# Performance work log

Measured on AMD Instinct MI355X. Metric: run time of the kernel, lower is better.

Reference implementation:

```python
import jax, jax.numpy as jnp
import numpy as np

N, E, G = 100000, 1600000, 64
IN_DIM, EMB, HID, HEADS, OUT = 128, 128, 32, 4, 64
CAT = HID * HEADS  # 128
EPS = 1e-5
SLOPE = 0.2


def gat_conv(x, src, dst, W, a_src, a_dst, bias):
    # x: [N, F_in]; W: [HEADS*HID, F_in]; a_*: [1, HEADS, HID]; bias: [HEADS*HID]
    h = (x @ W.T).reshape(N, HEADS, HID)
    s_src = (h * a_src).sum(-1)  # [N, HEADS]
    s_dst = (h * a_dst).sum(-1)
    e = jax.nn.leaky_relu(s_src[src] + s_dst[dst], SLOPE)  # [Etot, HEADS]
    m = jax.ops.segment_max(e, dst, num_segments=N)
    p = jnp.exp(e - m[dst])
    denom = jax.ops.segment_sum(p, dst, num_segments=N)
    alpha = p / denom[dst]  # softmax over incoming edges per dst node
    out = jax.ops.segment_sum(h[src] * alpha[:, :, None], dst, num_segments=N)
    return out.reshape(N, CAT) + bias


def graph_norm(x, batch, w, b, mean_scale):
    cnt = jax.ops.segment_sum(jnp.ones((N,), x.dtype), batch, num_segments=G)[:, None]
    mean = jax.ops.segment_sum(x, batch, num_segments=G) / cnt  # [G, C]
    sub = x - mean_scale * mean[batch]
    var = jax.ops.segment_sum(sub * sub, batch, num_segments=G) / cnt
    inv = 1.0 / jnp.sqrt(var + EPS)
    return w * sub * inv[batch] + b


def setup_inputs() -> dict:
    key = jax.random.key(0)
    ks = jax.random.split(key, 20)
    g = lambda k, shape, s: jax.random.normal(k, shape, dtype=jnp.float32) * s
    inp = {
        'x': g(ks[0], (N, IN_DIM), 1.0),
        'edge_index': jax.random.randint(ks[1], (2, E), 0, N, dtype=jnp.int64 if jax.config.read('jax_enable_x64') else jnp.int32),
        'batch': jnp.sort(jax.random.randint(ks[2], (N,), 0, G)),
        'enc_w': g(ks[3], (EMB, IN_DIM), 0.08),
        'enc_b': jnp.zeros((EMB,), jnp.float32),
        'w1': g(ks[4], (HEADS * HID, EMB), 0.08),
        'att_src1': g(ks[5], (1, HEADS, HID), 0.15),
        'att_dst1': g(ks[6], (1, HEADS, HID), 0.15),
        'b1': jnp.zeros((CAT,), jnp.float32),
        'n1_w': jnp.ones((CAT,), jnp.float32),
        'n1_b': jnp.zeros((CAT,), jnp.float32),
        'n1_ms': jnp.ones((CAT,), jnp.float32),
        'w2': g(ks[7], (HEADS * HID, CAT), 0.08),
        'att_src2': g(ks[8], (1, HEADS, HID), 0.15),
        'att_dst2': g(ks[9], (1, HEADS, HID), 0.15),
        'b2': jnp.zeros((CAT,), jnp.float32),
        'n2_w': jnp.ones((CAT,), jnp.float32),
        'n2_b': jnp.zeros((CAT,), jnp.float32),
        'n2_ms': jnp.ones((CAT,), jnp.float32),
        'fc_w': g(ks[10], (OUT, CAT), 0.08),
        'fc_b': jnp.zeros((OUT,), jnp.float32),
    }
    return inp


def reference(x, edge_index, batch, enc_w, enc_b, w1, att_src1, att_dst1, b1,
              n1_w, n1_b, n1_ms, w2, att_src2, att_dst2, b2, n2_w, n2_b, n2_ms,
              fc_w, fc_b):
    # PyG GATConv adds self-loops by default
    loops = jnp.arange(N, dtype=edge_index.dtype)
    src = jnp.concatenate([edge_index[0], loops])
    dst = jnp.concatenate([edge_index[1], loops])

    h = x @ enc_w.T + enc_b
    h = jax.nn.elu(gat_conv(h, src, dst, w1, att_src1, att_dst1, b1))
    h = graph_norm(h, batch, n1_w, n1_b, n1_ms)  # dropout = identity (eval)
    h = jax.nn.elu(gat_conv(h, src, dst, w2, att_src2, att_dst2, b2))
    h = graph_norm(h, batch, n2_w, n2_b, n2_ms)
    pooled = jax.ops.segment_max(h, batch, num_segments=G)  # global_max_pool
    return pooled @ fc_w.T + fc_b  # out_dim != 1 -> no sigmoid
```

## Files before the change

kernel.cpp:

```cpp
#include <hip/hip_runtime.h>
#include <hip/hip_bf16.h>

#define SLOPE 0.2f
#define EPS_GN 1e-5f
#define APITCH 136
#define NBUCK 391

typedef __attribute__((ext_vector_type(8))) short bfrag;
typedef __attribute__((ext_vector_type(4))) float ffrag;

__device__ __forceinline__ float lrelu(float v) { return v > 0.f ? v : SLOPE * v; }
__device__ __forceinline__ unsigned int flipf(float x) {
    unsigned int u = __float_as_uint(x);
    return (u & 0x80000000u) ? ~u : (u | 0x80000000u);
}
__device__ __forceinline__ float unflipf(unsigned int u) {
    return __uint_as_float((u & 0x80000000u) ? (u & 0x7fffffffu) : ~u);
}
__device__ __forceinline__ short f2bs(float v) {
    __hip_bfloat16 h = __float2bfloat16(v);
    return *reinterpret_cast<short*>(&h);
}
__device__ __forceinline__ float bs2f(short s) {
    __hip_bfloat16 h = *reinterpret_cast<__hip_bfloat16*>(&s);
    return __bfloat162float(h);
}
__device__ __forceinline__ float blo(unsigned int u) { return __uint_as_float(u << 16); }
__device__ __forceinline__ float bhi(unsigned int u) { return __uint_as_float(u & 0xffff0000u); }

__global__ void zero_kernel(float* __restrict__ p, int n) {
    int i = blockIdx.x * 256 + threadIdx.x;
    if (i < n) p[i] = 0.f;
}

__global__ void prep_weights(const float* __restrict__ enc_w,
                             const float* __restrict__ enc_b,
                             const float* __restrict__ w1,
                             const float* __restrict__ w2,
                             unsigned short* __restrict__ WT1b,
                             unsigned short* __restrict__ WT2b,
                             float* __restrict__ bc1, float* __restrict__ bc2) {
    int c = blockIdx.x;
    int k = threadIdx.x;
    __shared__ float w1row[128];
    w1row[k] = w1[c * 128 + k];
    __syncthreads();
    float acc = 0.f;
    for (int j = 0; j < 128; ++j)
        acc = fmaf(w1row[j], enc_w[j * 128 + k], acc);
    WT1b[c * 128 + k] = (unsigned short)f2bs(acc);
    WT2b[c * 128 + k] = (unsigned short)f2bs(w2[c * 128 + k]);
    if (k == 0) {
        float b = 0.f;
        for (int j = 0; j < 128; ++j) b += w1row[j] * enc_b[j];
        bc1[c] = b;
        bc2[c] = 0.f;
    }
}


__global__ void __launch_bounds__(256) bucket_hist(const int* __restrict__ ei,
                                                   int* __restrict__ bhist, int E, int N) {
    __shared__ int h[NBUCK];
    for (int i = threadIdx.x; i < NBUCK; i += 256) h[i] = 0;
    __syncthreads();
    int base = blockIdx.x * 4096;
#pragma unroll
    for (int s = 0; s < 16; ++s) {
        int e = base + s * 256 + threadIdx.x;
        if (e < E + N) {
            int dst = (e < E) ? ei[E + e] : (e - E);
            atomicAdd(&h[dst >> 8], 1);
        }
    }
    __syncthreads();
    for (int i = threadIdx.x; i < NBUCK; i += 256)
        if (h[i]) atomicAdd(&bhist[i], h[i]);
}

__global__ void bucket_scan(const int* __restrict__ bhist,
                            int* __restrict__ bbase, int* __restrict__ bcur) {
    __shared__ int sh[512];
    int t = threadIdx.x;
    int v = (t < NBUCK) ? bhist[t] : 0;
    sh[t] = v;
    __syncthreads();
    for (int off = 1; off < 512; off <<= 1) {
        int add = (t >= off) ? sh[t - off] : 0;
        __syncthreads();
        sh[t] += add;
        __syncthreads();
    }
    if (t < NBUCK) {
        bbase[t] = sh[t] - v;
        bcur[t] = sh[t] - v;
    }
}

__global__ void __launch_bounds__(256) bucket_scatter(const int* __restrict__ ei,
                                                      int* __restrict__ bcur,
                                                      unsigned int* __restrict__ staging,
                                                      int E, int N) {
    __shared__ int h[NBUCK];
    __shared__ int lb[NBUCK];
    for (int i = threadIdx.x; i < NBUCK; i += 256) h[i] = 0;
    __syncthreads();
    int base = blockIdx.x * 4096;
    int srcv[16], dstv[16];
#pragma unroll
    for (int s = 0; s < 16; ++s) {
        int e = base + s * 256 + threadIdx.x;
        srcv[s] = -1;
        if (e < E + N) {
            srcv[s] = (e < E) ? ei[e] : (e - E);
            dstv[s] = (e < E) ? ei[E + e] : (e - E);
            atomicAdd(&h[dstv[s] >> 8], 1);
        }
    }
    __syncthreads();
    for (int i = threadIdx.x; i < NBUCK; i += 256) {
        int c = h[i];
        lb[i] = c ? atomicAdd(&bcur[i], c) : 0;
        h[i] = 0;
    }
    __syncthreads();
#pragma unroll
    for (int s = 0; s < 16; ++s) {
        if (srcv[s] >= 0) {
            int b = dstv[s] >> 8;
            int slot = atomicAdd(&h[b], 1);
            staging[lb[b] + slot] = ((unsigned int)srcv[s] << 8) | (unsigned int)(dstv[s] & 255);
        }
    }
}

__global__ void __launch_bounds__(256) bucket_deg(const unsigned int* __restrict__ staging,
                                                  const int* __restrict__ bbase,
                                                  const int* __restrict__ bcur,
                                                  int* __restrict__ deg, int N) {
    int b = blockIdx.x;
    __shared__ int h[256];
    h[threadIdx.x] = 0;
    __syncthreads();
    int s0 = bbase[b], s1 = bcur[b];
    for (int j = s0 + threadIdx.x; j < s1; j += 256)
        atomicAdd(&h[staging[j] & 255], 1);
    __syncthreads();
    int node = b * 256 + threadIdx.x;
    if (node < N) deg[node] = h[threadIdx.x];
}

__global__ void scan_block_sums(const int* __restrict__ deg, int* __restrict__ part, int N) {
    __shared__ int sh[256];
    int t = threadIdx.x;
    int i = blockIdx.x * 256 + t;
    sh[t] = (i < N) ? deg[i] : 0;
    __syncthreads();
    for (int off = 128; off; off >>= 1) {
        if (t < off) sh[t] += sh[t + off];
        __syncthreads();
    }
    if (t == 0) part[blockIdx.x] = sh[0];
}

__global__ void scan_partials(int* __restrict__ part, int nb) {
    __shared__ int sh[1024];
    int t = threadIdx.x;
    int v = (t < nb) ? part[t] : 0;
    sh[t] = v;
    __syncthreads();
    for (int off = 1; off < 1024; off <<= 1) {
        int add = (t >= off) ? sh[t - off] : 0;
        __syncthreads();
        sh[t] += add;
        __syncthreads();
    }
    if (t < nb) part[t] = sh[t] - v;
}

__global__ void scan_write(const int* __restrict__ deg, const int* __restrict__ part,
                           int* __restrict__ row, int N, int Etot) {
    __shared__ int sh[256];
    int t = threadIdx.x;
    int i = blockIdx.x * 256 + t;
    int v = (i < N) ? deg[i] : 0;
    sh[t] = v;
    __syncthreads();
    for (int off = 1; off < 256; off <<= 1) {
        int add = (t >= off) ? sh[t - off] : 0;
        __syncthreads();
        sh[t] += add;
        __syncthreads();
    }
    int excl = sh[t] - v + part[blockIdx.x];
    if (i < N) row[i] = excl;
    if (i == 0 && blockIdx.x == 0) row[N] = Etot;
}

__global__ void __launch_bounds__(256) bucket_csr(const unsigned int* __restrict__ staging,
                                                  const int* __restrict__ bbase,
                                                  const int* __restrict__ bcur,
                                                  const int* __restrict__ rowp,
                                                  int* __restrict__ esrc, int N) {
    int b = blockIdx.x;
    __shared__ int cur[256];
    int node = b * 256 + threadIdx.x;
    cur[threadIdx.x] = (node < N) ? rowp[node] : 0;
    __syncthreads();
    int s0 = bbase[b], s1 = bcur[b];
    for (int j = s0 + threadIdx.x; j < s1; j += 256) {
        unsigned int p = staging[j];
        int pos = atomicAdd(&cur[p & 255], 1);
        esrc[pos] = (int)(p >> 8);
    }
}

__global__ void __launch_bounds__(256) gemm_mfma(
    const void* __restrict__ Ain, const unsigned short* __restrict__ WTb,
    const float* __restrict__ bias, const float* __restrict__ att_src,
    const float* __restrict__ att_dst, const int* __restrict__ batch,
    const float* __restrict__ Ac, const float* __restrict__ Bc,
    unsigned int* __restrict__ H, float* __restrict__ ssrc, float* __restrict__ sdst, int N) {
    __shared__ short Bsh[128 * APITCH];
    __shared__ short Ash[64 * APITCH];
    __shared__ float asrc_s[128], adst_s[128], bias_s[128];
    int tid = threadIdx.x;
    int base = blockIdx.x * 64;

    for (int idx = tid; idx < 2048; idx += 256) {
        int c = idx >> 4, k8 = (idx & 15) * 8;
        uint4 wv = ((const uint4*)WTb)[idx];
        *(uint4*)&Bsh[c * APITCH + k8] = wv;
    }
    if (Ac == nullptr) {
        const float* A = (const float*)Ain;
        for (int idx = tid; idx < 2048; idx += 256) {
            int nl = idx >> 5, k4 = (idx & 31) * 4;
            int node = base + nl;
            float4 v = make_float4(0.f, 0.f, 0.f, 0.f);
            if (node < N) v = ((const float4*)A)[node * 32 + (idx & 31)];
            *(short4*)&Ash[nl * APITCH + k4] =
                make_short4(f2bs(v.x), f2bs(v.y), f2bs(v.z), f2bs(v.w));
        }
    } else {
        const uint4* A4 = (const uint4*)Ain;
        for (int idx = tid; idx < 1024; idx += 256) {
            int nl = idx >> 4, u4 = idx & 15, k8 = u4 * 8;
            int node = base + nl;
            short o[8] = {0, 0, 0, 0, 0, 0, 0, 0};
            if (node < N) {
                uint4 hb = A4[node * 16 + u4];
                int g = batch[node];
                float4 a0 = *(const float4*)&Ac[g * 128 + k8];
                float4 a1 = *(const float4*)&Ac[g * 128 + k8 + 4];
                float4 b0 = *(const float4*)&Bc[g * 128 + k8];
                float4 b1 = *(const float4*)&Bc[g * 128 + k8 + 4];
                o[0] = f2bs(fmaf(blo(hb.x), a0.x, b0.x));
                o[1] = f2bs(fmaf(bhi(hb.x), a0.y, b0.y));
                o[2] = f2bs(fmaf(blo(hb.y), a0.z, b0.z));
                o[3] = f2bs(fmaf(bhi(hb.y), a0.w, b0.w));
                o[4] = f2bs(fmaf(blo(hb.z), a1.x, b1.x));
                o[5] = f2bs(fmaf(bhi(hb.z), a1.y, b1.y));
                o[6] = f2bs(fmaf(blo(hb.w), a1.z, b1.z));
                o[7] = f2bs(fmaf(bhi(hb.w), a1.w, b1.w));
            }
            *(bfrag*)&Ash[nl * APITCH + k8] = *(bfrag*)o;
        }
    }
    if (tid < 128) {
        asrc_s[tid] = att_src[tid];
        adst_s[tid] = att_dst[tid];
        bias_s[tid] = bias[tid];
    }
    __syncthreads();

    int w = tid >> 6, lane = tid & 63, col = lane & 15, quad = lane >> 4;
    int rowBase = w * 16;

    bfrag afr[4];
#pragma unroll
    for (int s = 0; s < 4; ++s)
        afr[s] = *(const bfrag*)&Ash[(rowBase + col) * APITCH + s * 32 + quad * 8];

    ffrag acc[8];
#pragma unroll
    for (int t = 0; t < 8; ++t) acc[t] = (ffrag){0.f, 0.f, 0.f, 0.f};

#pragma unroll
    for (int t = 0; t < 8; ++t) {
#pragma unroll
        for (int s = 0; s < 4; ++s) {
            bfrag bfr = *(const bfrag*)&Bsh[(t * 16 + col) * APITCH + s * 32 + quad * 8];
            acc[t] = __builtin_amdgcn_mfma_f32_16x16x32_bf16(afr[s], bfr, acc[t], 0, 0, 0);
        }
    }

#pragma unroll
    for (int t = 0; t < 8; ++t) {
        int ch = t * 16 + col;
        float bv = bias_s[ch];
#pragma unroll
        for (int r = 0; r < 4; ++r)
            Ash[(rowBase + quad * 4 + r) * APITCH + ch] = f2bs(acc[t][r] + bv);
    }
    __syncthreads();

    float2 av = make_float2(asrc_s[lane * 2], asrc_s[lane * 2 + 1]);
    float2 dv = make_float2(adst_s[lane * 2], adst_s[lane * 2 + 1]);
    for (int r = 0; r < 16; ++r) {
        int node = base + rowBase + r;
        unsigned int hb = *(const unsigned int*)&Ash[(rowBase + r) * APITCH + lane * 2];
        float hx = blo(hb);
        float hy = bhi(hb);
        float vs = hx * av.x + hy * av.y;
        float vd = hx * dv.x + hy * dv.y;
#pragma unroll
        for (int off = 8; off; off >>= 1) {
            vs += __shfl_xor(vs, off, 16);
            vd += __shfl_xor(vd, off, 16);
        }
        if (node < N) {
            H[node * 64 + lane] = hb;
            if ((lane & 15) == 0) {
                int h = lane >> 4;
                ssrc[node * 4 + h] = vs;
                sdst[node * 4 + h] = vd;
            }
        }
    }
}

__global__ void __launch_bounds__(256) agg_kernel(
    const int* __restrict__ row, const int* __restrict__ esrc,
    const float* __restrict__ ssrc, const float* __restrict__ sdst,
    const uint4* __restrict__ H4, const float* __restrict__ bias,
    uint4* __restrict__ out, int N) {
    int n = (blockIdx.x * 256 + threadIdx.x) >> 6;
    int lane = threadIdx.x & 63;
    if (n >= N) return;
    int slot = lane >> 4, li = lane & 15, head = li >> 2;
    int beg = row[n], end = row[n + 1];
    float sdh = sdst[n * 4 + head];

    float num[8] = {0.f, 0.f, 0.f, 0.f, 0.f, 0.f, 0.f, 0.f};
    float den = 0.f;
    for (int e = beg + slot; e < end; e += 4) {
        int s = esrc[e];
        float al = __expf(lrelu(ssrc[s * 4 + head] + sdh));
        uint4 hb = H4[s * 16 + li];
        den += al;
        num[0] = fmaf(al, blo(hb.x), num[0]);
        num[1] = fmaf(al, bhi(hb.x), num[1]);
        num[2] = fmaf(al, blo(hb.y), num[2]);
        num[3] = fmaf(al, bhi(hb.y), num[3]);
        num[4] = fmaf(al, blo(hb.z), num[4]);
        num[5] = fmaf(al, bhi(hb.z), num[5]);
        num[6] = fmaf(al, blo(hb.w), num[6]);
        num[7] = fmaf(al, bhi(hb.w), num[7]);
    }
    den += __shfl_xor(den, 16);
    den += __shfl_xor(den, 32);
#pragma unroll
    for (int j = 0; j < 8; ++j) {
        num[j] += __shfl_xor(num[j], 16);
        num[j] += __shfl_xor(num[j], 32);
    }
    if (slot == 0) {
        float rh = 1.f / den;
        int c0 = li * 8;
        unsigned int o[4];
#pragma unroll
        for (int p = 0; p < 4; ++p) {
            float v0 = fmaf(num[2 * p], rh, bias[c0 + 2 * p]);
            float v1 = fmaf(num[2 * p + 1], rh, bias[c0 + 2 * p + 1]);
            v0 = v0 > 0.f ? v0 : __expf(v0) - 1.f;
            v1 = v1 > 0.f ? v1 : __expf(v1) - 1.f;
            o[p] = ((unsigned int)(unsigned short)f2bs(v0)) |
                   (((unsigned int)(unsigned short)f2bs(v1)) << 16);
        }
        out[n * 16 + li] = make_uint4(o[0], o[1], o[2], o[3]);
    }
}

__global__ void norm_stats(const short* __restrict__ X, const int* __restrict__ batch,
                           float* __restrict__ gsum, float* __restrict__ gsq,
                           int* __restrict__ gcnt, int N, int countFlag) {
    int c = threadIdx.x;
    int base = blockIdx.x * 64;
    if (base >= N) return;
    int end = min(base + 64, N);
    int cur = batch[base];
    float s = 0.f, q = 0.f;
    int cnt = 0;
    for (int n = base; n < end; ++n) {
        int g = batch[n];
        if (g != cur) {
            atomicAdd(&gsum[cur * 128 + c], s);
            atomicAdd(&gsq[cur * 128 + c], q);
            if (c == 0 && countFlag) atomicAdd(&gcnt[cur], cnt);
            s = 0.f; q = 0.f; cnt = 0; cur = g;
        }
        float v = bs2f(X[n * 128 + c]);
        s += v;
        q += v * v;
        ++cnt;
    }
    atomicAdd(&gsum[cur * 128 + c], s);
    atomicAdd(&gsq[cur * 128 + c], q);
    if (c == 0 && countFlag) atomicAdd(&gcnt[cur], cnt);
}

__global__ void norm_coef(const float* __restrict__ gsum, const float* __restrict__ gsq,
                          const int* __restrict__ gcnt,
                          const float* __restrict__ w, const float* __restrict__ b,
                          const float* __restrict__ ms,
                          float* __restrict__ Ac, float* __restrict__ Bc) {
    int g = blockIdx.x, c = threadIdx.x;
    int i = g * 128 + c;
    float cntv = (float)gcnt[g];
    if (cntv < 0.5f) { Ac[i] = 0.f; Bc[i] = 0.f; return; }
    float mean = gsum[i] / cntv;
    float msv = ms[c];
    float var = gsq[i] / cntv - msv * (2.f - msv) * mean * mean;
    var = fmaxf(var, 0.f);
    float inv = rsqrtf(var + EPS_GN);
    float wv = w[c];
    Ac[i] = wv * inv;
    Bc[i] = b[c] - msv * mean * wv * inv;
}

__global__ void norm_pool(const short* __restrict__ X, const int* __restrict__ batch,
                          const float* __restrict__ Ac, const float* __restrict__ Bc,
                          unsigned int* __restrict__ pool, int N) {
    int c = threadIdx.x;
    int base = blockIdx.x * 64;
    if (base >= N) return;
    int end = min(base + 64, N);
    int cur = batch[base];
    float mx = -3e38f;
    for (int n = base; n < end; ++n) {
        int g = batch[n];
        if (g != cur) {
            atomicMax(&pool[cur * 128 + c], flipf(mx));
            mx = -3e38f;
            cur = g;
        }
        float v = fmaf(bs2f(X[n * 128 + c]), Ac[g * 128 + c], Bc[g * 128 + c]);
        mx = fmaxf(mx, v);
    }
    atomicMax(&pool[cur * 128 + c], flipf(mx));
}

__global__ void fc_kernel(const unsigned int* __restrict__ pool,
                          const float* __restrict__ fcw,
                          const float* __restrict__ fcb,
                          float* __restrict__ out) {
    int g = blockIdx.x, o = threadIdx.x;
    __shared__ float p[128];
    p[o] = unflipf(pool[g * 128 + o]);
    p[o + 64] = unflipf(pool[g * 128 + 64 + o]);
    __syncthreads();
    float acc = fcb[o];
    for (int k = 0; k < 128; ++k)
        acc = fmaf(p[k], fcw[o * 128 + k], acc);
    out[g * 64 + o] = acc;
}

extern "C" void kernel_launch(void* const* d_in, const int* in_sizes, int n_in,
                              void* d_out, int out_size, void* d_ws, size_t ws_size,
                              hipStream_t stream) {
    const float* x     = (const float*)d_in[0];
    const int* ei      = (const int*)d_in[1];
    const int* batch   = (const int*)d_in[2];
    const float* enc_w = (const float*)d_in[3];
    const float* enc_b = (const float*)d_in[4];
    const float* w1    = (const float*)d_in[5];
    const float* as1   = (const float*)d_in[6];
    const float* ad1   = (const float*)d_in[7];
    const float* b1    = (const float*)d_in[8];
    const float* n1w   = (const float*)d_in[9];
    const float* n1b   = (const float*)d_in[10];
    const float* n1ms  = (const float*)d_in[11];
    const float* w2    = (const float*)d_in[12];
    const float* as2   = (const float*)d_in[13];
    const float* ad2   = (const float*)d_in[14];
    const float* b2    = (const float*)d_in[15];
    const float* n2w   = (const float*)d_in[16];
    const float* n2b   = (const float*)d_in[17];
    const float* n2ms  = (const float*)d_in[18];
    const float* fcw   = (const float*)d_in[19];
    const float* fcb   = (const float*)d_in[20];
    float* out = (float*)d_out;

    int N = in_sizes[2];
    int E = in_sizes[1] / 2;
    int Etot = E + N;

    char* ws = (char*)d_ws;
    size_t off = 0;
    auto take = [&](size_t bytes) {
        char* p = ws + off;
        off = (off + bytes + 255) & ~(size_t)255;
        return p;
    };
    unsigned short* WT1b = (unsigned short*)take(128 * 128 * 2);
    unsigned short* WT2b = (unsigned short*)take(128 * 128 * 2);
    float* bc1 = (float*)take(512);
    float* bc2 = (float*)take(512);
    float* ssrc = (float*)take((size_t)N * 16);
    float* sdst = (float*)take((size_t)N * 16);
    int* rowp   = (int*)take((size_t)(N + 1) * 4);
    int* part   = (int*)take(4096 * 4);
    int* esrc   = (int*)take((size_t)Etot * 4);
    unsigned int* staging = (unsigned int*)take((size_t)Etot * 4);
    int* bbase  = (int*)take(512 * 4);
    int* bcur   = (int*)take(512 * 4);
    int* deg    = (int*)take((size_t)N * 4);
    unsigned int* H = (unsigned int*)take((size_t)N * 256);
    unsigned int* AG = (unsigned int*)take((size_t)N * 256);
    float* Ac   = (float*)take(64 * 128 * 4);
    float* Bc   = (float*)take(64 * 128 * 4);
    size_t zbeg = off;
    int* bhist   = (int*)take(512 * 4);
    float* gsumA = (float*)take(64 * 128 * 4);
    float* gsqA  = (float*)take(64 * 128 * 4);
    float* gsumB = (float*)take(64 * 128 * 4);
    float* gsqB  = (float*)take(64 * 128 * 4);
    int* gcnt    = (int*)take(256);
    unsigned int* pool = (unsigned int*)take(64 * 128 * 4);
    size_t zend = off;
    if (off > ws_size) return;

    int zn = (int)((zend - zbeg) / 4);
    int NB = (N + 255) / 256;
    int EB = (Etot + 4095) / 4096;

    zero_kernel<<<(zn + 255) / 256, 256, 0, stream>>>((float*)(ws + zbeg), zn);
    prep_weights<<<128, 128, 0, stream>>>(enc_w, enc_b, w1, w2, WT1b, WT2b, bc1, bc2);

    bucket_hist<<<EB, 256, 0, stream>>>(ei, bhist, E, N);
    bucket_scan<<<1, 512, 0, stream>>>(bhist, bbase, bcur);
    bucket_scatter<<<EB, 256, 0, stream>>>(ei, bcur, staging, E, N);
    bucket_deg<<<NBUCK, 256, 0, stream>>>(staging, bbase, bcur, deg, N);
    scan_block_sums<<<NB, 256, 0, stream>>>(deg, part, N);
    scan_partials<<<1, 1024, 0, stream>>>(part, NB);
    scan_write<<<NB, 256, 0, stream>>>(deg, part, rowp, N, Etot);
    bucket_csr<<<NBUCK, 256, 0, stream>>>(staging, bbase, bcur, rowp, esrc, N);

    gemm_mfma<<<(N + 63) / 64, 256, 0, stream>>>(x, WT1b, bc1, as1, ad1, batch,
                                                 nullptr, nullptr, H, ssrc, sdst, N);
    agg_kernel<<<(N + 3) / 4, 256, 0, stream>>>(rowp, esrc, ssrc, sdst,
                                                (const uint4*)H, b1, (uint4*)AG, N);
    norm_stats<<<(N + 63) / 64, 128, 0, stream>>>((const short*)AG, batch, gsumA, gsqA, gcnt, N, 1);
    norm_coef<<<64, 128, 0, stream>>>(gsumA, gsqA, gcnt, n1w, n1b, n1ms, Ac, Bc);

    gemm_mfma<<<(N + 63) / 64, 256, 0, stream>>>(AG, WT2b, bc2, as2, ad2, batch,
                                                 Ac, Bc, H, ssrc, sdst, N);
    agg_kernel<<<(N + 3) / 4, 256, 0, stream>>>(rowp, esrc, ssrc, sdst,
                                                (const uint4*)H, b2, (uint4*)AG, N);
    norm_stats<<<(N + 63) / 64, 128, 0, stream>>>((const short*)AG, batch, gsumB, gsqB, gcnt, N, 0);
    norm_coef<<<64, 128, 0, stream>>>(gsumB, gsqB, gcnt, n2w, n2b, n2ms, Ac, Bc);
    norm_pool<<<(N + 63) / 64, 128, 0, stream>>>((const short*)AG, batch, Ac, Bc, pool, N);

    fc_kernel<<<64, 64, 0, stream>>>(pool, fcw, fcb, out);
}
```

Before: 483.8 us.

## Fuse CSR degree, scan and fill into one kernel; prefetch edges in aggregation

Combines the per-bucket degree count, the three-pass global prefix scan and the CSR fill into one kernel. It relies on each 256-node bucket's edges already sitting contiguously at bbase[b], so row offsets come from a local block scan. This removes four launches and the deg/part round trips through memory. Separately, the aggregation loop is software-pipelined: the next edge's source scores and features and the index two steps ahead are loaded before the current edge is accumulated, hiding gather latency at the cost of more registers.

```diff
diff --git a/kernel.cpp b/kernel.cpp
--- a/kernel.cpp
+++ b/kernel.cpp
@@ -134,83 +134,37 @@
     }
 }
 
-__global__ void __launch_bounds__(256) bucket_deg(const unsigned int* __restrict__ staging,
-                                                  const int* __restrict__ bbase,
-                                                  const int* __restrict__ bcur,
-                                                  int* __restrict__ deg, int N) {
-    int b = blockIdx.x;
-    __shared__ int h[256];
-    h[threadIdx.x] = 0;
+__global__ void __launch_bounds__(256) bucket_finalize(
+    const unsigned int* __restrict__ staging,
+    const int* __restrict__ bbase, const int* __restrict__ bcur,
+    int* __restrict__ rowp, int* __restrict__ esrc, int N, int Etot) {
+    int b = blockIdx.x, t = threadIdx.x;
+    __shared__ int h[256], sc[256];
+    h[t] = 0;
     __syncthreads();
     int s0 = bbase[b], s1 = bcur[b];
-    for (int j = s0 + threadIdx.x; j < s1; j += 256)
+    for (int j = s0 + t; j < s1; j += 256)
         atomicAdd(&h[staging[j] & 255], 1);
     __syncthreads();
-    int node = b * 256 + threadIdx.x;
-    if (node < N) deg[node] = h[threadIdx.x];
-}
-
-__global__ void scan_block_sums(const int* __restrict__ deg, int* __restrict__ part, int N) {
-    __shared__ int sh[256];
-    int t = threadIdx.x;
-    int i = blockIdx.x * 256 + t;
-    sh[t] = (i < N) ? deg[i] : 0;
-    __syncthreads();
-    for (int off = 128; off; off >>= 1) {
-        if (t < off) sh[t] += sh[t + off];
+    int d = h[t];
+    sc[t] = d;
+    __syncthreads();
+    for (int off = 1; off < 256; off <<= 1) {
+        int add = (t >= off) ? sc[t - off] : 0;
         __syncthreads();
-    }
-    if (t == 0) part[blockIdx.x] = sh[0];
-}
-
-__global__ void scan_partials(int* __restrict__ part, int nb) {
-    __shared__ int sh[1024];
-    int t = threadIdx.x;
-    int v = (t < nb) ? part[t] : 0;
-    sh[t] = v;
-    __syncthreads();
-    for (int off = 1; off < 1024; off <<= 1) {
-        int add = (t >= off) ? sh[t - off] : 0;
+        sc[t] += add;
         __syncthreads();
-        sh[t] += add;
-        __syncthreads();
-    }
-    if (t < nb) part[t] = sh[t] - v;
-}
-
-__global__ void scan_write(const int* __restrict__ deg, const int* __restrict__ part,
-                           int* __restrict__ row, int N, int Etot) {
-    __shared__ int sh[256];
-    int t = threadIdx.x;
-    int i = blockIdx.x * 256 + t;
-    int v = (i < N) ? deg[i] : 0;
-    sh[t] = v;
-    __syncthreads();
-    for (int off = 1; off < 256; off <<= 1) {
-        int add = (t >= off) ? sh[t - off] : 0;
-        __syncthreads();
-        sh[t] += add;
-        __syncthreads();
-    }
-    int excl = sh[t] - v + part[blockIdx.x];
-    if (i < N) row[i] = excl;
-    if (i == 0 && blockIdx.x == 0) row[N] = Etot;
-}
-
-__global__ void __launch_bounds__(256) bucket_csr(const unsigned int* __restrict__ staging,
-                                                  const int* __restrict__ bbase,
-                                                  const int* __restrict__ bcur,
-                                                  const int* __restrict__ rowp,
-                                                  int* __restrict__ esrc, int N) {
-    int b = blockIdx.x;
-    __shared__ int cur[256];
-    int node = b * 256 + threadIdx.x;
-    cur[threadIdx.x] = (node < N) ? rowp[node] : 0;
-    __syncthreads();
-    int s0 = bbase[b], s1 = bcur[b];
-    for (int j = s0 + threadIdx.x; j < s1; j += 256) {
+    }
+    int excl = s0 + sc[t] - d;
+    int node = b * 256 + t;
+    if (node < N) rowp[node] = excl;
+    if (b == 0 && t == 0) rowp[N] = Etot;
+    __syncthreads();
+    h[t] = excl;
+    __syncthreads();
+    for (int j = s0 + t; j < s1; j += 256) {
         unsigned int p = staging[j];
-        int pos = atomicAdd(&cur[p & 255], 1);
+        int pos = atomicAdd(&h[p & 255], 1);
         esrc[pos] = (int)(p >> 8);
     }
 }
@@ -340,23 +294,35 @@
     if (n >= N) return;
     int slot = lane >> 4, li = lane & 15, head = li >> 2;
     int beg = row[n], end = row[n + 1];
+    int last = end - 1;
     float sdh = sdst[n * 4 + head];
+    int e0 = beg + slot;
 
     float num[8] = {0.f, 0.f, 0.f, 0.f, 0.f, 0.f, 0.f, 0.f};
     float den = 0.f;
-    for (int e = beg + slot; e < end; e += 4) {
-        int s = esrc[e];
-        float al = __expf(lrelu(ssrc[s * 4 + head] + sdh));
-        uint4 hb = H4[s * 16 + li];
+
+    int sA = esrc[min(e0, last)];
+    float svA = ssrc[sA * 4 + head];
+    uint4 hbA = H4[sA * 16 + li];
+    int sB = esrc[min(e0 + 4, last)];
+
+    for (int e = e0; e < end; e += 4) {
+        float svB = ssrc[sB * 4 + head];
+        uint4 hbB = H4[sB * 16 + li];
+        int sC = esrc[min(e + 8, last)];
+        float al = __expf(lrelu(svA + sdh));
         den += al;
-        num[0] = fmaf(al, blo(hb.x), num[0]);
-        num[1] = fmaf(al, bhi(hb.x), num[1]);
-        num[2] = fmaf(al, blo(hb.y), num[2]);
-        num[3] = fmaf(al, bhi(hb.y), num[3]);
-        num[4] = fmaf(al, blo(hb.z), num[4]);
-        num[5] = fmaf(al, bhi(hb.z), num[5]);
-        num[6] = fmaf(al, blo(hb.w), num[6]);
-        num[7] = fmaf(al, bhi(hb.w), num[7]);
+        num[0] = fmaf(al, blo(hbA.x), num[0]);
+        num[1] = fmaf(al, bhi(hbA.x), num[1]);
+        num[2] = fmaf(al, blo(hbA.y), num[2]);
+        num[3] = fmaf(al, bhi(hbA.y), num[3]);
+        num[4] = fmaf(al, blo(hbA.z), num[4]);
+        num[5] = fmaf(al, bhi(hbA.z), num[5]);
+        num[6] = fmaf(al, blo(hbA.w), num[6]);
+        num[7] = fmaf(al, bhi(hbA.w), num[7]);
+        svA = svB;
+        hbA = hbB;
+        sB = sC;
     }
     den += __shfl_xor(den, 16);
     den += __shfl_xor(den, 32);
@@ -510,12 +476,10 @@
     float* ssrc = (float*)take((size_t)N * 16);
     float* sdst = (float*)take((size_t)N * 16);
     int* rowp   = (int*)take((size_t)(N + 1) * 4);
-    int* part   = (int*)take(4096 * 4);
     int* esrc   = (int*)take((size_t)Etot * 4);
     unsigned int* staging = (unsigned int*)take((size_t)Etot * 4);
     int* bbase  = (int*)take(512 * 4);
     int* bcur   = (int*)take(512 * 4);
-    int* deg    = (int*)take((size_t)N * 4);
     unsigned int* H = (unsigned int*)take((size_t)N * 256);
     unsigned int* AG = (unsigned int*)take((size_t)N * 256);
     float* Ac   = (float*)take(64 * 128 * 4);
@@ -532,7 +496,6 @@
     if (off > ws_size) return;
 
     int zn = (int)((zend - zbeg) / 4);
-    int NB = (N + 255) / 256;
     int EB = (Etot + 4095) / 4096;
 
     zero_kernel<<<(zn + 255) / 256, 256, 0, stream>>>((float*)(ws + zbeg), zn);
@@ -541,11 +504,7 @@
     bucket_hist<<<EB, 256, 0, stream>>>(ei, bhist, E, N);
     bucket_scan<<<1, 512, 0, stream>>>(bhist, bbase, bcur);
     bucket_scatter<<<EB, 256, 0, stream>>>(ei, bcur, staging, E, N);
-    bucket_deg<<<NBUCK, 256, 0, stream>>>(staging, bbase, bcur, deg, N);
-    scan_block_sums<<<NB, 256, 0, stream>>>(deg, part, N);
-    scan_partials<<<1, 1024, 0, stream>>>(part, NB);
-    scan_write<<<NB, 256, 0, stream>>>(deg, part, rowp, N, Etot);
-    bucket_csr<<<NBUCK, 256, 0, stream>>>(staging, bbase, bcur, rowp, esrc, N);
+    bucket_finalize<<<NBUCK, 256, 0, stream>>>(staging, bbase, bcur, rowp, esrc, N, Etot);
 
     gemm_mfma<<<(N + 63) / 64, 256, 0, stream>>>(x, WT1b, bc1, as1, ad1, batch,
                                                  nullptr, nullptr, H, ssrc, sdst, N);
```

New measurement: 472.3 us. 2.4% less time.
